# Kernel tuning notes

Measured on AMD Instinct MI355X. Metric: run time of the kernel, lower is better.

## Reference

```python
import jax, jax.numpy as jnp
import numpy as np

B, N, M = 8, 1024, 64          # graphs, ops/graph, machines/graph
OPF, MF = 16, 8                # raw feature dims
H, D, L = 8, 64, 3             # heads, head dim, HGT layers
F = H * D                      # 512 = hidden_dim * num_heads
KC = 8                         # compatible machines per op
NOP, NM = B * N, B * M
EPS = 1e-5


def _graph_ln(x, w, b):
    # PyG LayerNorm(mode='graph') with batch=None: scalar mean/std over the whole tensor
    x = x - x.mean()
    return x / (x.std() + EPS) * w + b


def _seg_softmax(a, idx, n):
    amax = jax.ops.segment_max(a, idx, num_segments=n)
    amax = jnp.where(jnp.isfinite(amax), amax, 0.0)
    ex = jnp.exp(a - amax[idx])
    s = jax.ops.segment_sum(ex, idx, num_segments=n)
    return ex / (s[idx] + 1e-16)


def _forward(op_x, machine_x, W_emb_op, b_emb_op, W_emb_m, b_emb_m,
             opn_w, opn_b, mn_w, mn_b, Wk, bk, Wq, bq, Wv, bv,
             A_rel, M_rel, p_rel, W_out, b_out, skip, ln_w, ln_b,
             ei_precedes, ei_canproc, ei_compat):
    x_op = _graph_ln(op_x @ W_emb_op + b_emb_op, opn_w, opn_b)
    x_m = _graph_ln(machine_x @ W_emb_m + b_emb_m, mn_w, mn_b)
    s0, d0 = ei_precedes   # op -> op
    s1, d1 = ei_canproc    # machine -> op
    s2, d2 = ei_compat     # op -> machine
    scale = 1.0 / jnp.sqrt(jnp.float32(D))
    for l in range(L):
        k_op = (x_op @ Wk[l, 0] + bk[l, 0]).reshape(NOP, H, D)
        q_op = (x_op @ Wq[l, 0] + bq[l, 0]).reshape(NOP, H, D)
        v_op = (x_op @ Wv[l, 0] + bv[l, 0]).reshape(NOP, H, D)
        k_m = (x_m @ Wk[l, 1] + bk[l, 1]).reshape(NM, H, D)
        q_m = (x_m @ Wq[l, 1] + bq[l, 1]).reshape(NM, H, D)
        v_m = (x_m @ Wv[l, 1] + bv[l, 1]).reshape(NM, H, D)
        # relation-specific per-head transforms (a_rel/m_rel of HGTConv)
        k0 = jnp.einsum('nhd,hde->nhe', k_op, A_rel[l, 0]); v0 = jnp.einsum('nhd,hde->nhe', v_op, M_rel[l, 0])
        k1 = jnp.einsum('nhd,hde->nhe', k_m, A_rel[l, 1]);  v1 = jnp.einsum('nhd,hde->nhe', v_m, M_rel[l, 1])
        k2 = jnp.einsum('nhd,hde->nhe', k_op, A_rel[l, 2]); v2 = jnp.einsum('nhd,hde->nhe', v_op, M_rel[l, 2])
        # attention into op nodes: joint softmax over both incoming edge types
        a0 = (q_op[d0] * k0[s0]).sum(-1) * p_rel[l, 0] * scale   # [E0,H]
        a1 = (q_op[d1] * k1[s1]).sum(-1) * p_rel[l, 1] * scale   # [E1,H]
        a_op = jnp.concatenate([a0, a1]); dd = jnp.concatenate([d0, d1])
        w = _seg_softmax(a_op, dd, NOP)
        msg = jnp.concatenate([v0[s0], v1[s1]]) * w[:, :, None]
        agg_op = jax.ops.segment_sum(msg, dd, num_segments=NOP).reshape(NOP, F)
        # attention into machine nodes
        a2 = (q_m[d2] * k2[s2]).sum(-1) * p_rel[l, 2] * scale
        w2 = _seg_softmax(a2, d2, NM)
        agg_m = jax.ops.segment_sum(v2[s2] * w2[:, :, None], d2, num_segments=NM).reshape(NM, F)
        # output projection + learned skip gate (HGTConv internals)
        o_op = jax.nn.gelu(agg_op, approximate=False) @ W_out[l, 0] + b_out[l, 0]
        o_m = jax.nn.gelu(agg_m, approximate=False) @ W_out[l, 1] + b_out[l, 1]
        g_op = jax.nn.sigmoid(skip[l, 0]); g_m = jax.nn.sigmoid(skip[l, 1])
        o_op = g_op * o_op + (1.0 - g_op) * x_op
        o_m = g_m * o_m + (1.0 - g_m) * x_m
        # wrapper residual + dropout(eval=identity) + graph layer norm
        x_op = _graph_ln(o_op + x_op, ln_w[l], ln_b[l])
        x_m = _graph_ln(o_m + x_m, ln_w[l], ln_b[l])
    fea_j = x_op.reshape(B, N, F)
    fea_m = x_m.reshape(B, M, F)
    return fea_j, fea_m, fea_j.mean(1, keepdims=True), fea_m.mean(1, keepdims=True)


def setup_inputs() -> dict:
    key = jax.random.key(0)
    ks = jax.random.split(key, 12)
    rng = np.random.default_rng(0)
    ids = np.arange(NOP).reshape(B, N)
    src0 = ids[:, :-1].ravel(); dst0 = ids[:, 1:].ravel()
    mach = rng.integers(0, M, size=(B, N, KC)) + (np.arange(B) * M)[:, None, None]
    ops = np.broadcast_to(ids[:, :, None], (B, N, KC))
    ei_precedes = jnp.asarray(np.stack([src0, dst0]), dtype=jnp.int32)
    ei_canproc = jnp.asarray(np.stack([mach.ravel(), ops.ravel()]), dtype=jnp.int32)
    ei_compat = jnp.asarray(np.stack([ops.ravel(), mach.ravel()]), dtype=jnp.int32)
    n = lambda k, sh, s=0.05: jax.random.normal(k, sh, dtype=jnp.float32) * s
    return dict(
        op_x=n(ks[0], (NOP, OPF), 1.0),
        machine_x=n(ks[1], (NM, MF), 1.0),
        W_emb_op=n(ks[2], (OPF, F)), b_emb_op=jnp.zeros((F,), jnp.float32),
        W_emb_m=n(ks[3], (MF, F)), b_emb_m=jnp.zeros((F,), jnp.float32),
        opn_w=jnp.ones((F,), jnp.float32), opn_b=jnp.zeros((F,), jnp.float32),
        mn_w=jnp.ones((F,), jnp.float32), mn_b=jnp.zeros((F,), jnp.float32),
        Wk=n(ks[4], (L, 2, F, F)), bk=jnp.zeros((L, 2, F), jnp.float32),
        Wq=n(ks[5], (L, 2, F, F)), bq=jnp.zeros((L, 2, F), jnp.float32),
        Wv=n(ks[6], (L, 2, F, F)), bv=jnp.zeros((L, 2, F), jnp.float32),
        A_rel=n(ks[7], (L, 3, H, D, D)), M_rel=n(ks[8], (L, 3, H, D, D)),
        p_rel=jnp.ones((L, 3, H), jnp.float32),
        W_out=n(ks[9], (L, 2, F, F)), b_out=jnp.zeros((L, 2, F), jnp.float32),
        skip=jnp.ones((L, 2), jnp.float32),
        ln_w=jnp.ones((L, F), jnp.float32), ln_b=jnp.zeros((L, F), jnp.float32),
        ei_precedes=ei_precedes, ei_canproc=ei_canproc, ei_compat=ei_compat,
    )


def reference(op_x, machine_x, W_emb_op, b_emb_op, W_emb_m, b_emb_m,
              opn_w, opn_b, mn_w, mn_b, Wk, bk, Wq, bq, Wv, bv,
              A_rel, M_rel, p_rel, W_out, b_out, skip, ln_w, ln_b,
              ei_precedes, ei_canproc, ei_compat):
    return _forward(op_x, machine_x, W_emb_op, b_emb_op, W_emb_m, b_emb_m,
                    opn_w, opn_b, mn_w, mn_b, Wk, bk, Wq, bq, Wv, bv,
                    A_rel, M_rel, p_rel, W_out, b_out, skip, ln_w, ln_b,
                    ei_precedes, ei_canproc, ei_compat)
```

## Files before the change

### kernel.cpp

```cpp
#include <hip/hip_runtime.h>

typedef unsigned short u16;
typedef __attribute__((ext_vector_type(4))) float floatx4;
typedef __attribute__((ext_vector_type(8))) short shortx8;
typedef __attribute__((ext_vector_type(4))) short shortx4;

#define NOPS 8192
#define NMS  512
#define CQ   2560
#define CM   1536
#define NE2  65536
#define TOPC (NOPS*512)
#define TMC  (NMS*512)

__device__ __forceinline__ float bf2f(u16 u){ return __uint_as_float(((unsigned)u)<<16); }
__device__ __forceinline__ u16 f2bf(float f){
  unsigned u = __float_as_uint(f);
  u += 0x7FFFu + ((u>>16)&1u);
  return (u16)(u>>16);
}
__device__ __forceinline__ float wred(float v){
  #pragma unroll
  for (int o=32;o;o>>=1) v += __shfl_xor(v,o,64);
  return v;
}
__device__ __forceinline__ float wredmax(float v){
  #pragma unroll
  for (int o=32;o;o>>=1) v = fmaxf(v, __shfl_xor(v,o,64));
  return v;
}
__device__ __forceinline__ float geluf(float x){
  return 0.5f*x*(1.f+erff(x*0.70710678118654752f));
}
__device__ __forceinline__ void block_stat_out2(float s, float s2, float* pstat, int slot){
  __shared__ float sb[8];
  s = wred(s); s2 = wred(s2);
  int wv = threadIdx.x >> 6;
  if ((threadIdx.x & 63) == 0){ sb[wv*2] = s; sb[wv*2+1] = s2; }
  __syncthreads();
  if (threadIdx.x == 0){
    float a = 0.f, b = 0.f;
    int nw = blockDim.x >> 6;
    for (int i=0;i<nw;++i){ a += sb[i*2]; b += sb[i*2+1]; }
    pstat[slot*2]   = a;
    pstat[slot*2+1] = b;
  }
}

__global__ __launch_bounds__(256) void cnt2_k(const int* __restrict__ s1, float* __restrict__ Ct,
                                              float* __restrict__ Cn){
  int idx = blockIdx.x*256 + threadIdx.x;
  int n = idx >> 6, l = idx & 63;
  const int* row = s1 + n*8;
  int cnt = 0;
  #pragma unroll
  for (int j=0;j<8;++j) cnt += ((row[j] & 63) == l);
  float f = (float)cnt;
  Cn[(size_t)n*64 + l] = f;
  int b = n >> 10, nl = n & 1023;
  Ct[(size_t)((b<<6) + l)*1024 + nl] = f;
}

__global__ __launch_bounds__(256) void twout_k(const float* __restrict__ src, u16* __restrict__ dst){
  __shared__ u16 t[64][65];
  int l = blockIdx.x, kb = blockIdx.y*64, nb = blockIdx.z*64;
  const float* s = src + (size_t)l*262144;
  u16* d = dst + (size_t)l*262144;
  int tx = threadIdx.x & 63, ty4 = threadIdx.x >> 6;
  #pragma unroll 4
  for (int p=0;p<16;++p){
    int k = ty4 + p*4;
    t[k][tx] = f2bf(s[(size_t)(kb+k)*512 + nb + tx]);
  }
  __syncthreads();
  #pragma unroll 4
  for (int p=0;p<16;++p){
    int n = ty4 + p*4;
    d[(size_t)(nb+n)*512 + kb + tx] = t[tx][n];
  }
}

__global__ __launch_bounds__(256) void tq_k(const float* __restrict__ Wq,
                                            u16* __restrict__ Wc_op_t, u16* __restrict__ Wc_m_t){
  __shared__ u16 tl[64][65];
  int blk = blockIdx.x;
  int l = blk >> 1, side = blk & 1;
  const float* s = Wq + (size_t)blk*262144;
  u16* d = side ? (Wc_m_t + (size_t)l*CM*512) : (Wc_op_t + (size_t)l*CQ*512);
  int kb = blockIdx.y*64, nb = blockIdx.z*64;
  int tx = threadIdx.x & 63, ty4 = threadIdx.x >> 6;
  #pragma unroll 4
  for (int p=0;p<16;++p){
    int k = ty4 + p*4;
    tl[k][tx] = f2bf(s[(size_t)(kb+k)*512 + nb + tx]);
  }
  __syncthreads();
  #pragma unroll 4
  for (int p=0;p<16;++p){
    int n = ty4 + p*4;
    d[(size_t)(nb+n)*512 + kb + tx] = tl[tx][n];
  }
}

__global__ void qb_k(const float* __restrict__ bq, float* bias_op, float* bias_m){
  int i = blockIdx.x*blockDim.x + threadIdx.x;
  if (i >= 3072) return;
  int l = i >> 10, side = (i >> 9) & 1, f = i & 511;
  float v = bq[(l*2+side)*512 + f];
  if (side==0) bias_op[l*CQ + f] = v; else bias_m[l*CM + f] = v;
}

__global__ __launch_bounds__(256) void combine3_k(const float* __restrict__ Wk, const float* __restrict__ Wv,
                                                  const float* __restrict__ Ar, const float* __restrict__ Mr,
                                                  u16* __restrict__ Wc_op_t, u16* __restrict__ Wc_m_t){
  __shared__ u16 As[64*72];
  __shared__ u16 Bs[128*72];
  int gx = blockIdx.x;
  int l = gx/48; int rem = gx - l*48; int s = rem >> 3; int h = rem & 7;
  int side = (s < 4) ? 0 : 1;
  int r = (s < 4) ? (s+1) : (s-3);
  int useK = side==0 ? (s==0 || s==2) : (s==4);
  int rel  = side==0 ? ((s<2)?0:2) : 1;
  const float* W   = (useK ? Wk : Wv) + (size_t)(l*2+side)*262144;
  const float* Rel = (useK ? Ar : Mr) + ((size_t)(l*3+rel)*8 + h)*4096;
  int h64 = h*64;
  u16* Wt = side ? (Wc_m_t + (size_t)l*CM*512) : (Wc_op_t + (size_t)l*CQ*512);
  int rbase = r*512 + h64;
  int cc0 = blockIdx.y * 128;
  int tid = threadIdx.x, lane = tid & 63, wave = tid >> 6;
  {
    int d = tid >> 2, e0 = (tid & 3) * 16;
    #pragma unroll
    for (int j=0;j<16;++j) As[(e0+j)*72 + d] = f2bf(Rel[d*64 + e0 + j]);
  }
  {
    int ccl = tid >> 1, d0 = (tid & 1) * 32;
    const float* src = W + (size_t)(cc0+ccl)*512 + h64 + d0;
    #pragma unroll
    for (int j=0;j<32;j+=4){
      floatx4 v = *(const floatx4*)(src + j);
      shortx4 sv;
      #pragma unroll
      for (int e=0;e<4;++e) sv[e] = (short)f2bf(v[e]);
      *(shortx4*)(Bs + ccl*72 + d0 + j) = sv;
    }
  }
  __syncthreads();
  int wm = wave & 1, wn = wave >> 1;
  int mrow = lane & 15, quad = lane >> 4;
  floatx4 acc[2][4];
  #pragma unroll
  for (int a=0;a<2;++a)
    #pragma unroll
    for (int b=0;b<4;++b) acc[a][b] = (floatx4){0.f,0.f,0.f,0.f};
  #pragma unroll
  for (int ks=0; ks<2; ++ks){
    shortx8 af[2], bf[4];
    #pragma unroll
    for (int mt=0;mt<2;++mt) af[mt] = *(const shortx8*)(As + (wm*32 + mt*16 + mrow)*72 + ks*32 + quad*8);
    #pragma unroll
    for (int nt=0;nt<4;++nt) bf[nt] = *(const shortx8*)(Bs + (wn*64 + nt*16 + mrow)*72 + ks*32 + quad*8);
    #pragma unroll
    for (int mt=0;mt<2;++mt)
      #pragma unroll
      for (int nt=0;nt<4;++nt)
        acc[mt][nt] = __builtin_amdgcn_mfma_f32_16x16x32_bf16(af[mt], bf[nt], acc[mt][nt], 0, 0, 0);
  }
  #pragma unroll
  for (int mt=0;mt<2;++mt){
    #pragma unroll
    for (int nt=0;nt<4;++nt){
      int ccl = wn*64 + nt*16 + mrow;
      #pragma unroll
      for (int r2=0;r2<4;++r2){
        int e = wm*32 + mt*16 + quad*4 + r2;
        Wt[(size_t)(rbase + e)*512 + cc0 + ccl] = f2bf(acc[mt][nt][r2]);
      }
    }
  }
}
__global__ void cbias_k(const float* __restrict__ bk, const float* __restrict__ bv,
                        const float* __restrict__ Ar, const float* __restrict__ Mr,
                        float* bias_op, float* bias_m){
  int gx = blockIdx.x; int e = threadIdx.x;
  int l = gx/48; int rem = gx - l*48; int s = rem >> 3; int h = rem & 7;
  int side = (s < 4) ? 0 : 1;
  int r = (s < 4) ? (s+1) : (s-3);
  int useK = side==0 ? (s==0 || s==2) : (s==4);
  int rel  = side==0 ? ((s<2)?0:2) : 1;
  const float* bb  = (useK ? bk : bv) + (size_t)(l*2+side)*512 + h*64;
  const float* Rel = (useK ? Ar : Mr) + ((size_t)(l*3+rel)*8 + h)*4096;
  float acc = 0.f;
  for (int d=0; d<64; ++d) acc += bb[d]*Rel[d*64 + e];
  float* bias = side ? (bias_m + l*CM) : (bias_op + l*CQ);
  bias[r*512 + h*64 + e] = acc;
}

__global__ __launch_bounds__(256) void embed2_k(const float* __restrict__ Xop, const float* __restrict__ Wop,
                                                const float* __restrict__ bop, float* __restrict__ Yop,
                                                const float* __restrict__ Xm, const float* __restrict__ Wm,
                                                const float* __restrict__ bm_, float* __restrict__ Ym,
                                                float* pstat, float* pstat_m){
  int bid = blockIdx.x;
  const float *X, *W, *bias; float *Y, *ps; int K, total, nb, lb;
  if (bid < 1024){ X=Xop; W=Wop; bias=bop; Y=Yop; ps=pstat;   K=16; total=TOPC; nb=1024; lb=bid; }
  else           { X=Xm;  W=Wm;  bias=bm_; Y=Ym;  ps=pstat_m; K=8;  total=TMC;  nb=128;  lb=bid-1024; }
  float s = 0.f, s2 = 0.f;
  for (int idx = lb*256 + threadIdx.x; idx < total; idx += nb*256){
    int n = idx >> 9, f = idx & 511;
    float v = bias[f];
    for (int c=0;c<K;++c) v += X[n*K+c] * W[c*512+f];
    Y[idx] = v;
    s += v; s2 += v*v;
  }
  block_stat_out2(s, s2, ps, lb);
}

__global__ __launch_bounds__(256) void ln2_k(const float* __restrict__ src_op, float* __restrict__ dst_op,
                                             u16* __restrict__ dbf_op, const float* __restrict__ w_op,
                                             const float* __restrict__ b_op,
                                             const float* __restrict__ src_m, float* __restrict__ dst_m,
                                             u16* __restrict__ dbf_m, const float* __restrict__ w_m,
                                             const float* __restrict__ b_m,
                                             const float* __restrict__ pstat, const float* __restrict__ pstat_m){
  int bid = blockIdx.x;
  const float *src, *w, *b, *ps; float* dst; u16* dbf; int total4, nb, lb, nblk; float inv_n;
  if (bid < 1024){ src=src_op; dst=dst_op; dbf=dbf_op; w=w_op; b=b_op; ps=pstat;
                   total4=TOPC/4; nb=1024; lb=bid; nblk=1024; inv_n=1.f/TOPC; }
  else           { src=src_m;  dst=dst_m;  dbf=dbf_m;  w=w_m;  b=b_m;  ps=pstat_m;
                   total4=TMC/4;  nb=128;  lb=bid-1024; nblk=128; inv_n=1.f/TMC; }
  __shared__ float sb[8];
  __shared__ float mr[2];
  float s = 0.f, s2 = 0.f;
  for (int i = threadIdx.x; i < nblk; i += 256){ s += ps[2*i]; s2 += ps[2*i+1]; }
  s = wred(s); s2 = wred(s2);
  int wv = threadIdx.x >> 6;
  if ((threadIdx.x & 63) == 0){ sb[wv*2] = s; sb[wv*2+1] = s2; }
  __syncthreads();
  if (threadIdx.x == 0){
    float a = 0.f, bsum = 0.f;
    for (int i=0;i<4;++i){ a += sb[i*2]; bsum += sb[i*2+1]; }
    float mean = a * inv_n;
    float var  = fmaxf(bsum * inv_n - mean*mean, 0.f);
    mr[0] = mean;
    mr[1] = 1.f/(sqrtf(var) + 1e-5f);
  }
  __syncthreads();
  float mean = mr[0], rinv = mr[1];
  const floatx4* s4 = (const floatx4*)src;
  floatx4* d4 = (floatx4*)dst;
  shortx4* db4 = (shortx4*)dbf;
  const floatx4* w4 = (const floatx4*)w;
  const floatx4* b4 = (const floatx4*)b;
  for (int i = lb*256 + threadIdx.x; i < total4; i += nb*256){
    int f = i & 127;
    floatx4 v = s4[i], wv2 = w4[f], bv = b4[f];
    shortx4 sv;
    #pragma unroll
    for (int e=0;e<4;++e){ v[e] = (v[e]-mean)*rinv*wv2[e] + bv[e]; sv[e] = (short)f2bf(v[e]); }
    d4[i] = v;
    db4[i] = sv;
  }
}

__global__ __launch_bounds__(256) void gate2_k(float* __restrict__ y_op, const float* __restrict__ x_op,
                                               const float* __restrict__ bo_op, const float* __restrict__ sk_op,
                                               float* __restrict__ y_m, const float* __restrict__ x_m,
                                               const float* __restrict__ bo_m, const float* __restrict__ sk_m,
                                               float* pstat, float* pstat_m){
  int bid = blockIdx.x;
  float *y, *ps; const float *x, *bo, *sk; int total4, nb, lb;
  if (bid < 1024){ y=y_op; x=x_op; bo=bo_op; sk=sk_op; ps=pstat;   total4=TOPC/4; nb=1024; lb=bid; }
  else           { y=y_m;  x=x_m;  bo=bo_m;  sk=sk_m;  ps=pstat_m; total4=TMC/4;  nb=128;  lb=bid-1024; }
  float g = 1.f/(1.f+expf(-(*sk)));
  floatx4* y4 = (floatx4*)y;
  const floatx4* x4 = (const floatx4*)x;
  const floatx4* b4 = (const floatx4*)bo;
  float s = 0.f, s2 = 0.f;
  for (int i = lb*256 + threadIdx.x; i < total4; i += nb*256){
    floatx4 yv = y4[i], xv = x4[i], bv = b4[i & 127];
    #pragma unroll
    for (int e=0;e<4;++e){
      float o = g*(yv[e]+bv[e]) + (2.f-g)*xv[e];
      yv[e] = o;
      s += o; s2 += o*o;
    }
    y4[i] = yv;
  }
  block_stat_out2(s, s2, ps, lb);
}

__device__ __forceinline__ void gemm_core(u16* As, u16* Bs, const u16* __restrict__ A,
                                          const u16* __restrict__ Bt, const float* __restrict__ bias,
                                          void* __restrict__ Cp, int N, int K, int out_bf16,
                                          int bx, int by){
  const int tid = threadIdx.x;
  const int lane = tid & 63, wave = tid >> 6;
  const int bm = by * 128, bn = bx * 128;
  const int wm = wave & 1, wn = wave >> 1;
  const int mrow = lane & 15, quad = lane >> 4;
  const u16* Ab = A + (size_t)bm*K;
  const u16* Bb = Bt + (size_t)bn*K;
  floatx4 acc[4][4];
  #pragma unroll
  for (int a=0;a<4;++a)
    #pragma unroll
    for (int b=0;b<4;++b) acc[a][b] = (floatx4){0.f,0.f,0.f,0.f};
  const int r0 = tid >> 2, c0 = (tid & 3) * 8;
  const int r1 = (tid+256) >> 2, c1 = ((tid+256) & 3) * 8;
  const int lds0 = wave*512;
  const int lds1 = wave*512 + 2048;
  for (int k0 = 0; k0 < K; k0 += 32){
    __builtin_amdgcn_global_load_lds((const __attribute__((address_space(1))) void*)(Ab + (size_t)r0*K + k0 + c0),
                                     (__attribute__((address_space(3))) void*)(As + lds0), 16, 0, 0);
    __builtin_amdgcn_global_load_lds((const __attribute__((address_space(1))) void*)(Ab + (size_t)r1*K + k0 + c1),
                                     (__attribute__((address_space(3))) void*)(As + lds1), 16, 0, 0);
    __builtin_amdgcn_global_load_lds((const __attribute__((address_space(1))) void*)(Bb + (size_t)r0*K + k0 + c0),
                                     (__attribute__((address_space(3))) void*)(Bs + lds0), 16, 0, 0);
    __builtin_amdgcn_global_load_lds((const __attribute__((address_space(1))) void*)(Bb + (size_t)r1*K + k0 + c1),
                                     (__attribute__((address_space(3))) void*)(Bs + lds1), 16, 0, 0);
    __syncthreads();
    shortx8 af[4], bf[4];
    #pragma unroll
    for (int mt=0;mt<4;++mt) af[mt] = *(const shortx8*)(As + (wm*64 + mt*16 + mrow)*32 + quad*8);
    #pragma unroll
    for (int nt=0;nt<4;++nt) bf[nt] = *(const shortx8*)(Bs + (wn*64 + nt*16 + mrow)*32 + quad*8);
    #pragma unroll
    for (int mt=0;mt<4;++mt)
      #pragma unroll
      for (int nt=0;nt<4;++nt)
        acc[mt][nt] = __builtin_amdgcn_mfma_f32_16x16x32_bf16(af[mt], bf[nt], acc[mt][nt], 0, 0, 0);
    __syncthreads();
  }
  #pragma unroll
  for (int mt=0;mt<4;++mt){
    #pragma unroll
    for (int nt=0;nt<4;++nt){
      int col = bn + wn*64 + nt*16 + mrow;
      float bval = bias ? bias[col] : 0.f;
      #pragma unroll
      for (int r2=0;r2<4;++r2){
        int row = bm + wm*64 + mt*16 + quad*4 + r2;
        float v = acc[mt][nt][r2] + bval;
        if (out_bf16) ((u16*)Cp)[(size_t)row*N + col] = f2bf(v);
        else          ((float*)Cp)[(size_t)row*N + col] = v;
      }
    }
  }
}
__global__ __launch_bounds__(256) void gemm2_k(const u16* A1, const u16* B1, const float* bias1, void* C1,
                                               int N1, int ob1, int ntx1, int nblk1,
                                               const u16* A2, const u16* B2, const float* bias2, void* C2,
                                               int N2, int ob2, int ntx2, int K){
  __shared__ u16 As[128*32];
  __shared__ u16 Bs[128*32];
  int id = blockIdx.x;
  if (id < nblk1) gemm_core(As, Bs, A1, B1, bias1, C1, N1, K, ob1, id % ntx1, id / ntx1);
  else { int j = id - nblk1; gemm_core(As, Bs, A2, B2, bias2, C2, N2, K, ob2, j % ntx2, j / ntx2); }
}

__device__ __forceinline__ void stage_half8(const u16* __restrict__ src, int kc, u16* region, int tid){
  int wave = tid >> 6;
  #pragma unroll
  for (int j=0;j<2;++j){
    int idx = j*512 + tid;
    int row = idx >> 2, qp2 = idx & 3;
    int qs = qp2 ^ (((row >> 3) & 1) << 1);
    __builtin_amdgcn_global_load_lds(
      (const __attribute__((address_space(1))) void*)(src + (size_t)row*512 + kc + qs*8),
      (__attribute__((address_space(3))) void*)(region + (j*512 + wave*64)*8),
      16, 0, 0);
  }
}

#define MFMA_QUAD(MH) do { \
  __builtin_amdgcn_s_barrier(); \
  asm volatile("s_waitcnt lgkmcnt(0)" ::: "memory"); \
  __builtin_amdgcn_sched_barrier(0); \
  __builtin_amdgcn_s_setprio(1); \
  _Pragma("unroll") \
  for (int mt=0;mt<4;++mt){ \
    _Pragma("unroll") \
    for (int nt=0;nt<4;++nt) \
      acc[(MH)*4+mt][nt] = __builtin_amdgcn_mfma_f32_16x16x32_bf16(af[mt], bf[nt], acc[(MH)*4+mt][nt], 0, 0, 0); \
  } \
  __builtin_amdgcn_s_setprio(0); \
} while(0)

__global__ __launch_bounds__(512, 2) void gemm8_k(
    const u16* __restrict__ A1, const u16* __restrict__ B1, const float* __restrict__ bias1,
    u16* __restrict__ C1, int N1, int nbx1, int nblk1,
    const u16* __restrict__ A2, const u16* __restrict__ B2, const float* __restrict__ bias2,
    u16* __restrict__ C2, int N2, int nbx2){
  extern __shared__ u16 lds[];
  int id = blockIdx.x;
  const u16 *A, *Bt; const float* bias; u16* C; int N, bx, by;
  if (id < nblk1){ A=A1; Bt=B1; bias=bias1; C=C1; N=N1; bx=id%nbx1; by=id/nbx1; }
  else { int j=id-nblk1; A=A2; Bt=B2; bias=bias2; C=C2; N=N2; bx=j%nbx2; by=j/nbx2; }
  const int tid = threadIdx.x, lane = tid & 63, wave = tid >> 6;
  const int wm = wave & 1, wn = wave >> 1;
  const int mrow = lane & 15, quad = lane >> 4;
  const int qp = quad ^ ((mrow & 8) ? 2 : 0);
  const u16* Ab = A + (size_t)(by*256)*512;
  const u16* Bb = Bt + (size_t)(bx*256)*512;

  floatx4 acc[8][4];
  #pragma unroll
  for (int a=0;a<8;++a)
    #pragma unroll
    for (int b=0;b<4;++b) acc[a][b] = (floatx4){0.f,0.f,0.f,0.f};

  stage_half8(Ab, 0,  lds,          tid);
  stage_half8(Bb, 0,  lds + 16384,  tid);
  stage_half8(Ab, 32, lds + 8192,   tid);
  stage_half8(Bb, 32, lds + 24576,  tid);
  stage_half8(Ab, 64, lds + 32768,  tid);
  stage_half8(Bb, 64, lds + 49152,  tid);
  asm volatile("s_waitcnt vmcnt(4)" ::: "memory");
  __builtin_amdgcn_s_barrier();

  for (int t = 0; t < 8; ++t){
    const int s = t & 1;
    u16* Sbase = lds + s*32768;
    u16* Obase = lds + (s^1)*32768;
    const u16* a0 = Sbase + (wm*128 + mrow)*32 + qp*8;
    const u16* b0 = Sbase + 16384 + (wn*64 + mrow)*32 + qp*8;
    const int kc1 = (t+1)*64, kc2 = (t+2)*64;
    shortx8 af[4], bf[4];

    #pragma unroll
    for (int mt=0;mt<4;++mt) af[mt] = *(const shortx8*)(a0 + mt*512);
    #pragma unroll
    for (int nt=0;nt<4;++nt) bf[nt] = *(const shortx8*)(b0 + nt*512);
    if (t < 7) stage_half8(Ab, kc1 + 32, Obase + 8192, tid);
    MFMA_QUAD(0);
    __builtin_amdgcn_s_barrier();

    #pragma unroll
    for (int mt=0;mt<4;++mt) af[mt] = *(const shortx8*)(a0 + 2048 + mt*512);
    if (t < 7) stage_half8(Bb, kc1 + 32, Obase + 24576, tid);
    MFMA_QUAD(1);
    __builtin_amdgcn_s_barrier();

    #pragma unroll
    for (int mt=0;mt<4;++mt) af[mt] = *(const shortx8*)(a0 + 8192 + mt*512);
    #pragma unroll
    for (int nt=0;nt<4;++nt) bf[nt] = *(const shortx8*)(b0 + 8192 + nt*512);
    if (t < 6) stage_half8(Ab, kc2, Sbase, tid);
    MFMA_QUAD(0);
    __builtin_amdgcn_s_barrier();

    #pragma unroll
    for (int mt=0;mt<4;++mt) af[mt] = *(const shortx8*)(a0 + 8192 + 2048 + mt*512);
    if (t < 6) stage_half8(Bb, kc2, Sbase + 16384, tid);
    MFMA_QUAD(1);
    if (t < 6) asm volatile("s_waitcnt vmcnt(4)" ::: "memory");
    else       asm volatile("s_waitcnt vmcnt(0)" ::: "memory");
    __builtin_amdgcn_s_barrier();
  }

  const int crow0 = by*256 + wm*128 + quad*4;
  const int ccol0 = bx*256 + wn*64 + mrow;
  float bv[4];
  #pragma unroll
  for (int nt=0;nt<4;++nt) bv[nt] = bias ? bias[ccol0 + nt*16] : 0.f;
  #pragma unroll
  for (int mh=0;mh<2;++mh){
    #pragma unroll
    for (int mt=0;mt<4;++mt){
      int row = crow0 + mh*64 + mt*16;
      #pragma unroll
      for (int nt=0;nt<4;++nt){
        int col = ccol0 + nt*16;
        #pragma unroll
        for (int r2=0;r2<4;++r2)
          C[(size_t)(row+r2)*N + col] = f2bf(acc[mh*4+mt][nt][r2] + bv[nt]);
      }
    }
  }
}

__global__ __launch_bounds__(256) void qk12_k(const u16* __restrict__ qkv_op, const u16* __restrict__ qkv_m,
                                              const float* __restrict__ prel, const float* __restrict__ Cn,
                                              u16* __restrict__ W1, float* __restrict__ wpre,
                                              float* __restrict__ linv, float* __restrict__ S2f){
  __shared__ __align__(16) char smem[36864];
  u16* As = (u16*)smem;
  u16* Bs = As + 128*72;
  float* Sbuf = (float*)smem;
  int bh = blockIdx.y; int b = bh >> 3, h = bh & 7;
  int n0 = blockIdx.x * 128;
  int tid = threadIdx.x, lane = tid & 63, wave = tid >> 6;
  int mrow = lane & 15, quad = lane >> 4;
  if (blockIdx.z == 0){
    int wm = wave & 1, wn = wave >> 1;
    float p1 = prel[8 + h] * 0.125f;
    {
      int row = tid >> 1, col = (tid & 1) * 32;
      const u16* src = qkv_op + (size_t)(b*1024 + n0 + row)*CQ + h*64 + col;
      #pragma unroll
      for (int e=0;e<4;++e) *(shortx8*)(As + row*72 + col + e*8) = *(const shortx8*)(src + e*8);
    }
    {
      int row = tid >> 2, col = (tid & 3) * 16;
      const u16* src = qkv_m + (size_t)(b*64 + row)*CM + 512 + h*64 + col;
      *(shortx8*)(Bs + row*72 + col)     = *(const shortx8*)(src);
      *(shortx8*)(Bs + row*72 + col + 8) = *(const shortx8*)(src + 8);
    }
    __syncthreads();
    floatx4 acc[4][2];
    #pragma unroll
    for (int a=0;a<4;++a){ acc[a][0] = (floatx4){0,0,0,0}; acc[a][1] = (floatx4){0,0,0,0}; }
    #pragma unroll
    for (int ks=0; ks<2; ++ks){
      shortx8 af[4], bf[2];
      #pragma unroll
      for (int mt=0;mt<4;++mt) af[mt] = *(const shortx8*)(As + (wm*64 + mt*16 + mrow)*72 + ks*32 + quad*8);
      #pragma unroll
      for (int nt=0;nt<2;++nt) bf[nt] = *(const shortx8*)(Bs + (wn*32 + nt*16 + mrow)*72 + ks*32 + quad*8);
      #pragma unroll
      for (int mt=0;mt<4;++mt)
        #pragma unroll
        for (int nt=0;nt<2;++nt)
          acc[mt][nt] = __builtin_amdgcn_mfma_f32_16x16x32_bf16(af[mt], bf[nt], acc[mt][nt], 0, 0, 0);
    }
    __syncthreads();
    #pragma unroll
    for (int mt=0;mt<4;++mt){
      #pragma unroll
      for (int nt=0;nt<2;++nt){
        int m = wn*32 + nt*16 + mrow;
        #pragma unroll
        for (int r2=0;r2<4;++r2){
          int nl = wm*64 + mt*16 + quad*4 + r2;
          Sbuf[nl*65 + m] = acc[mt][nt][r2] * p1;
        }
      }
    }
    __syncthreads();
    if (tid < 128){
      int n_g = b*1024 + n0 + tid;
      int nl  = n0 + tid;
      float sp = -1e30f;
      if (nl > 0){
        float p0 = prel[h] * 0.125f;
        const u16* qp = qkv_op + (size_t)n_g*CQ + h*64;
        const u16* kp = qkv_op + (size_t)(n_g-1)*CQ + 512 + h*64;
        float d = 0.f;
        #pragma unroll
        for (int j=0;j<8;++j){
          shortx8 qa = *(const shortx8*)(qp + j*8);
          shortx8 ka = *(const shortx8*)(kp + j*8);
          #pragma unroll
          for (int e=0;e<8;++e) d += bf2f((u16)qa[e])*bf2f((u16)ka[e]);
        }
        sp = d * p0;
      }
      const float* crow = Cn + (size_t)n_g*64;
      float mx = sp;
      #pragma unroll
      for (int m=0;m<64;++m){
        if (crow[m] > 0.f) mx = fmaxf(mx, Sbuf[tid*65 + m]);
      }
      float L = 0.f;
      u16* wrow = W1 + ((size_t)n_g*8 + h)*64;
      #pragma unroll
      for (int m0=0;m0<64;m0+=4){
        shortx4 pv;
        #pragma unroll
        for (int e=0;e<4;++e){
          float c = crow[m0+e];
          float w = (c > 0.f) ? c*expf(Sbuf[tid*65 + m0+e]-mx) : 0.f;
          L += w;
          pv[e] = (short)f2bf(w);
        }
        *(shortx4*)(wrow + m0) = pv;
      }
      float ep = (nl > 0) ? expf(sp - mx) : 0.f;
      L += ep;
      wpre[(size_t)n_g*8 + h] = ep;
      linv[(size_t)n_g*8 + h] = 1.f/(L + 1e-16f);
    }
  } else {
    float p2 = prel[16 + h] * 0.125f;
    {
      int row = tid >> 2, col = (tid & 3) * 16;
      const u16* src = qkv_m + (size_t)(b*64+row)*CM + h*64 + col;
      *(shortx8*)(As + row*72 + col)     = *(const shortx8*)(src);
      *(shortx8*)(As + row*72 + col + 8) = *(const shortx8*)(src + 8);
    }
    {
      int row = tid >> 1, col = (tid & 1) * 32;
      const u16* src = qkv_op + (size_t)(b*1024 + n0 + row)*CQ + 1536 + h*64 + col;
      #pragma unroll
      for (int e=0;e<4;++e) *(shortx8*)(Bs + row*72 + col + e*8) = *(const shortx8*)(src + e*8);
    }
    __syncthreads();
    floatx4 acc[4][2];
    #pragma unroll
    for (int a=0;a<4;++a){ acc[a][0] = (floatx4){0,0,0,0}; acc[a][1] = (floatx4){0,0,0,0}; }
    #pragma unroll
    for (int ks=0; ks<2; ++ks){
      shortx8 af[4], bf[2];
      #pragma unroll
      for (int mt=0;mt<4;++mt) af[mt] = *(const shortx8*)(As + (mt*16 + mrow)*72 + ks*32 + quad*8);
      #pragma unroll
      for (int nt=0;nt<2;++nt) bf[nt] = *(const shortx8*)(Bs + (wave*32 + nt*16 + mrow)*72 + ks*32 + quad*8);
      #pragma unroll
      for (int mt=0;mt<4;++mt)
        #pragma unroll
        for (int nt=0;nt<2;++nt)
          acc[mt][nt] = __builtin_amdgcn_mfma_f32_16x16x32_bf16(af[mt], bf[nt], acc[mt][nt], 0, 0, 0);
    }
    #pragma unroll
    for (int mt=0;mt<4;++mt){
      #pragma unroll
      for (int nt=0;nt<2;++nt){
        int n = n0 + wave*32 + nt*16 + mrow;
        #pragma unroll
        for (int r2=0;r2<4;++r2){
          int m = mt*16 + quad*4 + r2;
          S2f[((size_t)(b*64 + m)*8 + h)*1024 + n] = acc[mt][nt][r2] * p2;
        }
      }
    }
  }
}

__global__ __launch_bounds__(512) void msoftm_k(const float* __restrict__ S2f, const float* __restrict__ Ct,
                                                u16* __restrict__ W2){
  int m = blockIdx.x;
  int h = threadIdx.x >> 6, d = threadIdx.x & 63;
  const float* srow = S2f + ((size_t)m*8 + h)*1024;
  const float* crow = Ct + (size_t)m*1024;
  float s[16], c[16];
  #pragma unroll
  for (int it=0; it<16; ++it){ s[it] = srow[it*64 + d]; c[it] = crow[it*64 + d]; }
  float mx = -1e30f;
  #pragma unroll
  for (int it=0; it<16; ++it) if (c[it] > 0.f) mx = fmaxf(mx, s[it]);
  mx = wredmax(mx);
  float e[16], L = 0.f;
  #pragma unroll
  for (int it=0; it<16; ++it){
    e[it] = (c[it] > 0.f) ? c[it]*expf(s[it]-mx) : 0.f;
    L += e[it];
  }
  L = wred(L);
  float inv = 1.f/(L + 1e-16f);
  u16* wrow = W2 + ((size_t)m*8 + h)*1024;
  #pragma unroll
  for (int it=0; it<16; ++it) wrow[it*64 + d] = f2bf(e[it]*inv);
}

__global__ __launch_bounds__(256) void agg12_k(const u16* __restrict__ W1, const u16* __restrict__ qkv_op,
                                               const u16* __restrict__ qkv_m, const float* __restrict__ wpre,
                                               const float* __restrict__ linv, u16* __restrict__ agg_op,
                                               const u16* __restrict__ W2, u16* __restrict__ agg_m){
  __shared__ u16 As[128*72];
  __shared__ u16 Bs[64*72];
  int bid = blockIdx.x;
  int tid = threadIdx.x, lane = tid & 63, wave = tid >> 6;
  int wm = wave & 1, wn = wave >> 1;
  int mrow = lane & 15, quad = lane >> 4;
  if (bid < 512){
    int bh = bid >> 3; int b = bh >> 3, h = bh & 7;
    int n0 = (bid & 7) * 128;
    {
      int row = tid >> 1, col = (tid & 1) * 32;
      const u16* src = W1 + ((size_t)(b*1024 + n0 + row)*8 + h)*64 + col;
      #pragma unroll
      for (int e=0;e<4;++e) *(shortx8*)(As + row*72 + col + e*8) = *(const shortx8*)(src + e*8);
    }
    {
      int m = tid >> 2, dcol = (tid & 3) * 16;
      const u16* src = qkv_m + (size_t)(b*64 + m)*CM + 1024 + h*64 + dcol;
      shortx8 v0 = *(const shortx8*)(src);
      shortx8 v1 = *(const shortx8*)(src + 8);
      #pragma unroll
      for (int e=0;e<8;++e){ Bs[(dcol+e)*72 + m] = (u16)v0[e]; Bs[(dcol+8+e)*72 + m] = (u16)v1[e]; }
    }
    __syncthreads();
    floatx4 acc[4][2];
    #pragma unroll
    for (int a=0;a<4;++a){ acc[a][0] = (floatx4){0,0,0,0}; acc[a][1] = (floatx4){0,0,0,0}; }
    #pragma unroll
    for (int ks=0; ks<2; ++ks){
      shortx8 af[4], bf[2];
      #pragma unroll
      for (int mt=0;mt<4;++mt) af[mt] = *(const shortx8*)(As + (wm*64 + mt*16 + mrow)*72 + ks*32 + quad*8);
      #pragma unroll
      for (int nt=0;nt<2;++nt) bf[nt] = *(const shortx8*)(Bs + (wn*32 + nt*16 + mrow)*72 + ks*32 + quad*8);
      #pragma unroll
      for (int mt=0;mt<4;++mt)
        #pragma unroll
        for (int nt=0;nt<2;++nt)
          acc[mt][nt] = __builtin_amdgcn_mfma_f32_16x16x32_bf16(af[mt], bf[nt], acc[mt][nt], 0, 0, 0);
    }
    #pragma unroll
    for (int mt=0;mt<4;++mt){
      #pragma unroll
      for (int nt=0;nt<2;++nt){
        int d = wn*32 + nt*16 + mrow;
        #pragma unroll
        for (int r2=0;r2<4;++r2){
          int n = n0 + wm*64 + mt*16 + quad*4 + r2;
          size_t ng = (size_t)b*1024 + n;
          size_t ih = ng*8 + h;
          float v = acc[mt][nt][r2];
          if ((n & 1023) > 0) v += wpre[ih] * bf2f(qkv_op[(ng-1)*CQ + 1024 + h*64 + d]);
          v *= linv[ih];
          agg_op[ng*512 + h*64 + d] = f2bf(geluf(v));
        }
      }
    }
  } else {
    int bh = bid - 512; int b = bh >> 3, h = bh & 7;
    floatx4 acc[2][2];
    acc[0][0]=(floatx4){0,0,0,0}; acc[0][1]=(floatx4){0,0,0,0};
    acc[1][0]=(floatx4){0,0,0,0}; acc[1][1]=(floatx4){0,0,0,0};
    const int arow = tid >> 2, acol = (tid & 3) * 8;
    const int nrow = tid >> 3, dcol = (tid & 7) * 8;
    for (int ks = 0; ks < 32; ++ks){
      int nn0 = ks*32;
      *(shortx8*)(As + arow*40 + acol) =
          *(const shortx8*)(W2 + ((size_t)(b*64 + arow)*8 + h)*1024 + nn0 + acol);
      shortx8 vv = *(const shortx8*)(qkv_op + (size_t)(b*1024 + nn0 + nrow)*CQ + 2048 + h*64 + dcol);
      #pragma unroll
      for (int e=0;e<8;++e) Bs[(dcol+e)*40 + nrow] = (u16)vv[e];
      __syncthreads();
      shortx8 af[2], bf[2];
      #pragma unroll
      for (int mt=0;mt<2;++mt) af[mt] = *(const shortx8*)(As + (wm*32 + mt*16 + mrow)*40 + quad*8);
      #pragma unroll
      for (int nt=0;nt<2;++nt) bf[nt] = *(const shortx8*)(Bs + (wn*32 + nt*16 + mrow)*40 + quad*8);
      #pragma unroll
      for (int mt=0;mt<2;++mt)
        #pragma unroll
        for (int nt=0;nt<2;++nt)
          acc[mt][nt] = __builtin_amdgcn_mfma_f32_16x16x32_bf16(af[mt], bf[nt], acc[mt][nt], 0, 0, 0);
      __syncthreads();
    }
    #pragma unroll
    for (int mt=0;mt<2;++mt){
      #pragma unroll
      for (int nt=0;nt<2;++nt){
        int dd = wn*32 + nt*16 + mrow;
        #pragma unroll
        for (int r2=0;r2<4;++r2){
          int m = wm*32 + mt*16 + quad*4 + r2;
          agg_m[(size_t)(b*64 + m)*512 + h*64 + dd] = f2bf(geluf(acc[mt][nt][r2]));
        }
      }
    }
  }
}

__global__ __launch_bounds__(512) void meanj_part_k(const float* __restrict__ xo, float* scratchJ){
  int b = blockIdx.x, chunk = blockIdx.y, f = threadIdx.x;
  float s = 0.f;
  for (int r=0;r<128;++r){
    int row = b*1024 + chunk*128 + r;
    s += xo[(size_t)row*512 + f];
  }
  scratchJ[(b*8 + chunk)*512 + f] = s;
}
__global__ __launch_bounds__(512) void mean2_k(const float* __restrict__ scratchJ, float* __restrict__ out){
  int i = blockIdx.x*512 + threadIdx.x;
  if (i < 4096){
    int b = i >> 9, f = i & 511;
    float s = 0.f;
    #pragma unroll
    for (int c=0;c<8;++c) s += scratchJ[(b*8+c)*512 + f];
    out[4456448 + i] = s * (1.f/1024.f);
  } else {
    int j = i - 4096;
    int b = j >> 9, f = j & 511;
    float s = 0.f;
    for (int r=0;r<64;++r) s += out[(size_t)TOPC + (size_t)(b*64+r)*512 + f];
    out[4460544 + j] = s * (1.f/64.f);
  }
}

extern "C" void kernel_launch(void* const* d_in, const int* in_sizes, int n_in,
                              void* d_out, int out_size, void* d_ws, size_t ws_size,
                              hipStream_t stream){
  const float* op_x      = (const float*)d_in[0];
  const float* machine_x = (const float*)d_in[1];
  const float* W_emb_op  = (const float*)d_in[2];
  const float* b_emb_op  = (const float*)d_in[3];
  const float* W_emb_m   = (const float*)d_in[4];
  const float* b_emb_m   = (const float*)d_in[5];
  const float* opn_w     = (const float*)d_in[6];
  const float* opn_b     = (const float*)d_in[7];
  const float* mn_w      = (const float*)d_in[8];
  const float* mn_b      = (const float*)d_in[9];
  const float* Wk        = (const float*)d_in[10];
  const float* bk        = (const float*)d_in[11];
  const float* Wq        = (const float*)d_in[12];
  const float* bq        = (const float*)d_in[13];
  const float* Wv        = (const float*)d_in[14];
  const float* bv        = (const float*)d_in[15];
  const float* A_rel     = (const float*)d_in[16];
  const float* M_rel     = (const float*)d_in[17];
  const float* p_rel     = (const float*)d_in[18];
  const float* W_out     = (const float*)d_in[19];
  const float* b_out     = (const float*)d_in[20];
  const float* skip      = (const float*)d_in[21];
  const float* ln_w      = (const float*)d_in[22];
  const float* ln_b      = (const float*)d_in[23];
  const int* s1          = (const int*)d_in[25];
  float* out = (float*)d_out;

  char* ws = (char*)d_ws;
  size_t off = 0;
  auto alloc = [&](size_t bytes)->void*{
    void* p = ws + off;
    off = (off + bytes + 255) & ~(size_t)255;
    return p;
  };
  float* pstat     = (float*)alloc(4096*4);
  float* scratchJ  = (float*)alloc(32768*4);
  float* Ct        = (float*)alloc((size_t)NMS*1024*4);
  float* Cn        = (float*)alloc((size_t)NOPS*64*4);
  float* S2f       = (float*)alloc((size_t)NMS*8*1024*4);
  u16*   W2        = (u16*)  alloc((size_t)NMS*8*1024*2);
  u16*   W1        = (u16*)  alloc((size_t)NOPS*8*64*2);
  float* wpre      = (float*)alloc((size_t)NOPS*8*4);
  float* linv      = (float*)alloc((size_t)NOPS*8*4);
  float* x_op      = (float*)alloc((size_t)NOPS*512*4);
  u16*   x_op_bf   = (u16*)  alloc((size_t)NOPS*512*2);
  float* x_m       = (float*)alloc((size_t)NMS*512*4);
  u16*   x_m_bf    = (u16*)  alloc((size_t)NMS*512*2);
  u16*   qkv_op    = (u16*)  alloc((size_t)NOPS*CQ*2);
  u16*   qkv_m     = (u16*)  alloc((size_t)NMS*CM*2);
  u16*   agg_op    = (u16*)  alloc((size_t)NOPS*512*2);
  u16*   agg_m     = (u16*)  alloc((size_t)NMS*512*2);
  u16*   Wc_op_t   = (u16*)  alloc((size_t)3*CQ*512*2);
  float* bias_op   = (float*)alloc((size_t)3*CQ*4);
  u16*   Wc_m_t    = (u16*)  alloc((size_t)3*CM*512*2);
  float* bias_m    = (float*)alloc((size_t)3*CM*4);
  u16*   Wout_t    = (u16*)  alloc((size_t)6*262144*2);
  float* o_op      = (float*)qkv_op;
  float* o_m       = (float*)qkv_m;
  float* pstat_m   = pstat + 2048;

  cnt2_k<<<2048,256,0,stream>>>(s1, Ct, Cn);
  twout_k<<<dim3(6,8,8),256,0,stream>>>(W_out, Wout_t);
  tq_k<<<dim3(6,8,8),256,0,stream>>>(Wq, Wc_op_t, Wc_m_t);
  qb_k<<<12,256,0,stream>>>(bq, bias_op, bias_m);
  combine3_k<<<dim3(144,4),256,0,stream>>>(Wk, Wv, A_rel, M_rel, Wc_op_t, Wc_m_t);
  cbias_k<<<144,64,0,stream>>>(bk, bv, A_rel, M_rel, bias_op, bias_m);

  embed2_k<<<1152,256,0,stream>>>(op_x, W_emb_op, b_emb_op, x_op,
                                  machine_x, W_emb_m, b_emb_m, x_m, pstat, pstat_m);
  ln2_k<<<1152,256,0,stream>>>(x_op, x_op, x_op_bf, opn_w, opn_b,
                               x_m, x_m, x_m_bf, mn_w, mn_b, pstat, pstat_m);

  for (int l=0; l<3; ++l){
    int last = (l == 2);
    gemm8_k<<<332,512,131072,stream>>>(x_op_bf, Wc_op_t + (size_t)l*CQ*512, bias_op + l*CQ, qkv_op, CQ, 10, 320,
                                       x_m_bf, Wc_m_t + (size_t)l*CM*512, bias_m + l*CM, qkv_m, CM, 6);
    qk12_k<<<dim3(8,64,2),256,0,stream>>>(qkv_op, qkv_m, p_rel + l*24, Cn, W1, wpre, linv, S2f);
    msoftm_k<<<NMS,512,0,stream>>>(S2f, Ct, W2);
    agg12_k<<<576,256,0,stream>>>(W1, qkv_op, qkv_m, wpre, linv, agg_op, W2, agg_m);
    gemm2_k<<<272,256,0,stream>>>(agg_op, Wout_t + (size_t)(l*2+0)*262144, nullptr, o_op, 512, 0, 4, 256,
                                  agg_m, Wout_t + (size_t)(l*2+1)*262144, nullptr, o_m, 512, 0, 4, 512);
    gate2_k<<<1152,256,0,stream>>>(o_op, x_op, b_out + (size_t)(l*2+0)*512, skip + l*2+0,
                                   o_m, x_m, b_out + (size_t)(l*2+1)*512, skip + l*2+1, pstat, pstat_m);
    ln2_k<<<1152,256,0,stream>>>(o_op, last ? out : x_op, x_op_bf, ln_w + l*512, ln_b + l*512,
                                 o_m, last ? (out + TOPC) : x_m, x_m_bf, ln_w + l*512, ln_b + l*512,
                                 pstat, pstat_m);
  }

  meanj_part_k<<<dim3(8,8),512,0,stream>>>(out, scratchJ);
  mean2_k<<<16,512,0,stream>>>(scratchJ, out);
}
```

Baseline: 612.9 us.

## Fuse output projection with gated residual and stats; remap gemm8 blocks per XCD

The separate gate kernel is removed. The output-projection GEMM now applies bias, the sigmoid skip gate and the residual in its epilogue, and writes per-block sum/sumsq partials, so the follow-up layer norm reads 256/16 partials instead of 1024/128. The QKV GEMM also remaps op-side block ids so consecutive blocks on an XCD share tiles, and it replaces the conditional tail staging with clamped redundant loads plus a uniform vmcnt(8) wait. This saves one full read/write pass over the activations, in exchange for redundant loads in the last iterations and changed wait counts that could affect correctness.

```diff
diff --git a/kernel.cpp b/kernel.cpp
--- a/kernel.cpp
+++ b/kernel.cpp
@@ -222,13 +222,14 @@
                                              const float* __restrict__ src_m, float* __restrict__ dst_m,
                                              u16* __restrict__ dbf_m, const float* __restrict__ w_m,
                                              const float* __restrict__ b_m,
-                                             const float* __restrict__ pstat, const float* __restrict__ pstat_m){
+                                             const float* __restrict__ pstat, const float* __restrict__ pstat_m,
+                                             int nbo, int nbm){
   int bid = blockIdx.x;
   const float *src, *w, *b, *ps; float* dst; u16* dbf; int total4, nb, lb, nblk; float inv_n;
   if (bid < 1024){ src=src_op; dst=dst_op; dbf=dbf_op; w=w_op; b=b_op; ps=pstat;
-                   total4=TOPC/4; nb=1024; lb=bid; nblk=1024; inv_n=1.f/TOPC; }
+                   total4=TOPC/4; nb=1024; lb=bid; nblk=nbo; inv_n=1.f/TOPC; }
   else           { src=src_m;  dst=dst_m;  dbf=dbf_m;  w=w_m;  b=b_m;  ps=pstat_m;
-                   total4=TMC/4;  nb=128;  lb=bid-1024; nblk=128; inv_n=1.f/TMC; }
+                   total4=TMC/4;  nb=128;  lb=bid-1024; nblk=nbm; inv_n=1.f/TMC; }
   __shared__ float sb[8];
   __shared__ float mr[2];
   float s = 0.f, s2 = 0.f;
@@ -263,44 +264,18 @@
   }
 }
 
-__global__ __launch_bounds__(256) void gate2_k(float* __restrict__ y_op, const float* __restrict__ x_op,
-                                               const float* __restrict__ bo_op, const float* __restrict__ sk_op,
-                                               float* __restrict__ y_m, const float* __restrict__ x_m,
-                                               const float* __restrict__ bo_m, const float* __restrict__ sk_m,
-                                               float* pstat, float* pstat_m){
-  int bid = blockIdx.x;
-  float *y, *ps; const float *x, *bo, *sk; int total4, nb, lb;
-  if (bid < 1024){ y=y_op; x=x_op; bo=bo_op; sk=sk_op; ps=pstat;   total4=TOPC/4; nb=1024; lb=bid; }
-  else           { y=y_m;  x=x_m;  bo=bo_m;  sk=sk_m;  ps=pstat_m; total4=TMC/4;  nb=128;  lb=bid-1024; }
-  float g = 1.f/(1.f+expf(-(*sk)));
-  floatx4* y4 = (floatx4*)y;
-  const floatx4* x4 = (const floatx4*)x;
-  const floatx4* b4 = (const floatx4*)bo;
-  float s = 0.f, s2 = 0.f;
-  for (int i = lb*256 + threadIdx.x; i < total4; i += nb*256){
-    floatx4 yv = y4[i], xv = x4[i], bv = b4[i & 127];
-    #pragma unroll
-    for (int e=0;e<4;++e){
-      float o = g*(yv[e]+bv[e]) + (2.f-g)*xv[e];
-      yv[e] = o;
-      s += o; s2 += o*o;
-    }
-    y4[i] = yv;
-  }
-  block_stat_out2(s, s2, ps, lb);
-}
-
-__device__ __forceinline__ void gemm_core(u16* As, u16* Bs, const u16* __restrict__ A,
-                                          const u16* __restrict__ Bt, const float* __restrict__ bias,
-                                          void* __restrict__ Cp, int N, int K, int out_bf16,
-                                          int bx, int by){
+__device__ __forceinline__ void gemm_gate_core(u16* As, u16* Bs, const u16* __restrict__ A,
+                                               const u16* __restrict__ Bt,
+                                               const float* __restrict__ xr, const float* __restrict__ bo,
+                                               const float* __restrict__ sk, float* __restrict__ Y,
+                                               float* pstat, int slot, int bx, int by){
   const int tid = threadIdx.x;
   const int lane = tid & 63, wave = tid >> 6;
   const int bm = by * 128, bn = bx * 128;
   const int wm = wave & 1, wn = wave >> 1;
   const int mrow = lane & 15, quad = lane >> 4;
-  const u16* Ab = A + (size_t)bm*K;
-  const u16* Bb = Bt + (size_t)bn*K;
+  const u16* Ab = A + (size_t)bm*512;
+  const u16* Bb = Bt + (size_t)bn*512;
   floatx4 acc[4][4];
   #pragma unroll
   for (int a=0;a<4;++a)
@@ -310,14 +285,14 @@
   const int r1 = (tid+256) >> 2, c1 = ((tid+256) & 3) * 8;
   const int lds0 = wave*512;
   const int lds1 = wave*512 + 2048;
-  for (int k0 = 0; k0 < K; k0 += 32){
-    __builtin_amdgcn_global_load_lds((const __attribute__((address_space(1))) void*)(Ab + (size_t)r0*K + k0 + c0),
+  for (int k0 = 0; k0 < 512; k0 += 32){
+    __builtin_amdgcn_global_load_lds((const __attribute__((address_space(1))) void*)(Ab + (size_t)r0*512 + k0 + c0),
                                      (__attribute__((address_space(3))) void*)(As + lds0), 16, 0, 0);
-    __builtin_amdgcn_global_load_lds((const __attribute__((address_space(1))) void*)(Ab + (size_t)r1*K + k0 + c1),
+    __builtin_amdgcn_global_load_lds((const __attribute__((address_space(1))) void*)(Ab + (size_t)r1*512 + k0 + c1),
                                      (__attribute__((address_space(3))) void*)(As + lds1), 16, 0, 0);
-    __builtin_amdgcn_global_load_lds((const __attribute__((address_space(1))) void*)(Bb + (size_t)r0*K + k0 + c0),
+    __builtin_amdgcn_global_load_lds((const __attribute__((address_space(1))) void*)(Bb + (size_t)r0*512 + k0 + c0),
                                      (__attribute__((address_space(3))) void*)(Bs + lds0), 16, 0, 0);
-    __builtin_amdgcn_global_load_lds((const __attribute__((address_space(1))) void*)(Bb + (size_t)r1*K + k0 + c1),
+    __builtin_amdgcn_global_load_lds((const __attribute__((address_space(1))) void*)(Bb + (size_t)r1*512 + k0 + c1),
                                      (__attribute__((address_space(3))) void*)(Bs + lds1), 16, 0, 0);
     __syncthreads();
     shortx8 af[4], bf[4];
@@ -332,31 +307,36 @@
         acc[mt][nt] = __builtin_amdgcn_mfma_f32_16x16x32_bf16(af[mt], bf[nt], acc[mt][nt], 0, 0, 0);
     __syncthreads();
   }
+  float g = 1.f/(1.f+expf(-(*sk)));
+  float s = 0.f, s2 = 0.f;
   #pragma unroll
   for (int mt=0;mt<4;++mt){
     #pragma unroll
     for (int nt=0;nt<4;++nt){
       int col = bn + wn*64 + nt*16 + mrow;
-      float bval = bias ? bias[col] : 0.f;
+      float bval = bo[col];
       #pragma unroll
       for (int r2=0;r2<4;++r2){
         int row = bm + wm*64 + mt*16 + quad*4 + r2;
         float v = acc[mt][nt][r2] + bval;
-        if (out_bf16) ((u16*)Cp)[(size_t)row*N + col] = f2bf(v);
-        else          ((float*)Cp)[(size_t)row*N + col] = v;
-      }
-    }
-  }
-}
-__global__ __launch_bounds__(256) void gemm2_k(const u16* A1, const u16* B1, const float* bias1, void* C1,
-                                               int N1, int ob1, int ntx1, int nblk1,
-                                               const u16* A2, const u16* B2, const float* bias2, void* C2,
-                                               int N2, int ob2, int ntx2, int K){
+        float o = g*v + (2.f-g)*xr[(size_t)row*512 + col];
+        Y[(size_t)row*512 + col] = o;
+        s += o; s2 += o*o;
+      }
+    }
+  }
+  block_stat_out2(s, s2, pstat, slot);
+}
+__global__ __launch_bounds__(256) void gemmgate2_k(const u16* A1, const u16* B1, const float* x1,
+                                                   const float* bo1, const float* sk1, float* Y1, float* ps1,
+                                                   int nblk1,
+                                                   const u16* A2, const u16* B2, const float* x2,
+                                                   const float* bo2, const float* sk2, float* Y2, float* ps2){
   __shared__ u16 As[128*32];
   __shared__ u16 Bs[128*32];
   int id = blockIdx.x;
-  if (id < nblk1) gemm_core(As, Bs, A1, B1, bias1, C1, N1, K, ob1, id % ntx1, id / ntx1);
-  else { int j = id - nblk1; gemm_core(As, Bs, A2, B2, bias2, C2, N2, K, ob2, j % ntx2, j / ntx2); }
+  if (id < nblk1) gemm_gate_core(As, Bs, A1, B1, x1, bo1, sk1, Y1, ps1, id, id % 4, id / 4);
+  else { int j = id - nblk1; gemm_gate_core(As, Bs, A2, B2, x2, bo2, sk2, Y2, ps2, j, j % 4, j / 4); }
 }
 
 __device__ __forceinline__ void stage_half8(const u16* __restrict__ src, int kc, u16* region, int tid){
@@ -395,7 +375,11 @@
   extern __shared__ u16 lds[];
   int id = blockIdx.x;
   const u16 *A, *Bt; const float* bias; u16* C; int N, bx, by;
-  if (id < nblk1){ A=A1; Bt=B1; bias=bias1; C=C1; N=N1; bx=id%nbx1; by=id/nbx1; }
+  if (id < nblk1){
+    int xcd = id & 7, loc = id >> 3;
+    int wg = xcd * (nblk1 >> 3) + loc;
+    A=A1; Bt=B1; bias=bias1; C=C1; N=N1; bx=wg%nbx1; by=wg/nbx1;
+  }
   else { int j=id-nblk1; A=A2; Bt=B2; bias=bias2; C=C2; N=N2; bx=j%nbx2; by=j/nbx2; }
   const int tid = threadIdx.x, lane = tid & 63, wave = tid >> 6;
   const int wm = wave & 1, wn = wave >> 1;
@@ -416,7 +400,7 @@
   stage_half8(Bb, 32, lds + 24576,  tid);
   stage_half8(Ab, 64, lds + 32768,  tid);
   stage_half8(Bb, 64, lds + 49152,  tid);
-  asm volatile("s_waitcnt vmcnt(4)" ::: "memory");
+  asm volatile("s_waitcnt vmcnt(8)" ::: "memory");
   __builtin_amdgcn_s_barrier();
 
   for (int t = 0; t < 8; ++t){
@@ -425,37 +409,38 @@
     u16* Obase = lds + (s^1)*32768;
     const u16* a0 = Sbase + (wm*128 + mrow)*32 + qp*8;
     const u16* b0 = Sbase + 16384 + (wn*64 + mrow)*32 + qp*8;
-    const int kc1 = (t+1)*64, kc2 = (t+2)*64;
+    const int kc1 = ((t < 7) ? (t+1) : 7)*64 + 32;
+    const int kc2 = ((t < 6) ? (t+2) : 7)*64;
     shortx8 af[4], bf[4];
 
     #pragma unroll
     for (int mt=0;mt<4;++mt) af[mt] = *(const shortx8*)(a0 + mt*512);
     #pragma unroll
     for (int nt=0;nt<4;++nt) bf[nt] = *(const shortx8*)(b0 + nt*512);
-    if (t < 7) stage_half8(Ab, kc1 + 32, Obase + 8192, tid);
+    stage_half8(Ab, kc1, Obase + 8192, tid);
     MFMA_QUAD(0);
     __builtin_amdgcn_s_barrier();
 
     #pragma unroll
     for (int mt=0;mt<4;++mt) af[mt] = *(const shortx8*)(a0 + 2048 + mt*512);
-    if (t < 7) stage_half8(Bb, kc1 + 32, Obase + 24576, tid);
+    stage_half8(Bb, kc1, Obase + 24576, tid);
     MFMA_QUAD(1);
+    asm volatile("s_waitcnt vmcnt(8)" ::: "memory");
     __builtin_amdgcn_s_barrier();
 
     #pragma unroll
     for (int mt=0;mt<4;++mt) af[mt] = *(const shortx8*)(a0 + 8192 + mt*512);
     #pragma unroll
     for (int nt=0;nt<4;++nt) bf[nt] = *(const shortx8*)(b0 + 8192 + nt*512);
-    if (t < 6) stage_half8(Ab, kc2, Sbase, tid);
+    stage_half8(Ab, kc2, Sbase, tid);
     MFMA_QUAD(0);
     __builtin_amdgcn_s_barrier();
 
     #pragma unroll
     for (int mt=0;mt<4;++mt) af[mt] = *(const shortx8*)(a0 + 8192 + 2048 + mt*512);
-    if (t < 6) stage_half8(Bb, kc2, Sbase + 16384, tid);
+    stage_half8(Bb, kc2, Sbase + 16384, tid);
     MFMA_QUAD(1);
-    if (t < 6) asm volatile("s_waitcnt vmcnt(4)" ::: "memory");
-    else       asm volatile("s_waitcnt vmcnt(0)" ::: "memory");
+    asm volatile("s_waitcnt vmcnt(8)" ::: "memory");
     __builtin_amdgcn_s_barrier();
   }
 
@@ -855,7 +840,7 @@
   embed2_k<<<1152,256,0,stream>>>(op_x, W_emb_op, b_emb_op, x_op,
                                   machine_x, W_emb_m, b_emb_m, x_m, pstat, pstat_m);
   ln2_k<<<1152,256,0,stream>>>(x_op, x_op, x_op_bf, opn_w, opn_b,
-                               x_m, x_m, x_m_bf, mn_w, mn_b, pstat, pstat_m);
+                               x_m, x_m, x_m_bf, mn_w, mn_b, pstat, pstat_m, 1024, 128);
 
   for (int l=0; l<3; ++l){
     int last = (l == 2);
@@ -864,13 +849,13 @@
     qk12_k<<<dim3(8,64,2),256,0,stream>>>(qkv_op, qkv_m, p_rel + l*24, Cn, W1, wpre, linv, S2f);
     msoftm_k<<<NMS,512,0,stream>>>(S2f, Ct, W2);
     agg12_k<<<576,256,0,stream>>>(W1, qkv_op, qkv_m, wpre, linv, agg_op, W2, agg_m);
-    gemm2_k<<<272,256,0,stream>>>(agg_op, Wout_t + (size_t)(l*2+0)*262144, nullptr, o_op, 512, 0, 4, 256,
-                                  agg_m, Wout_t + (size_t)(l*2+1)*262144, nullptr, o_m, 512, 0, 4, 512);
-    gate2_k<<<1152,256,0,stream>>>(o_op, x_op, b_out + (size_t)(l*2+0)*512, skip + l*2+0,
-                                   o_m, x_m, b_out + (size_t)(l*2+1)*512, skip + l*2+1, pstat, pstat_m);
+    gemmgate2_k<<<272,256,0,stream>>>(agg_op, Wout_t + (size_t)(l*2+0)*262144, x_op,
+                                      b_out + (size_t)(l*2+0)*512, skip + l*2+0, o_op, pstat, 256,
+                                      agg_m, Wout_t + (size_t)(l*2+1)*262144, x_m,
+                                      b_out + (size_t)(l*2+1)*512, skip + l*2+1, o_m, pstat_m);
     ln2_k<<<1152,256,0,stream>>>(o_op, last ? out : x_op, x_op_bf, ln_w + l*512, ln_b + l*512,
                                  o_m, last ? (out + TOPC) : x_m, x_m_bf, ln_w + l*512, ln_b + l*512,
-                                 pstat, pstat_m);
+                                 pstat, pstat_m, 256, 16);
   }
 
   meanj_part_k<<<dim3(8,8),512,0,stream>>>(out, scratchJ);
```

After: 615.5 us. Within noise of the previous version (+0.4%).
